# Optimization experiments

Hardware: AMD Instinct MI355X
Metric: run time of the kernel (lower is better)

The kernel has to match this reference:

```python
import jax, jax.numpy as jnp
import numpy as np

N_EMBD = 384
HEAD_SIZE = 16

def setup_inputs() -> dict:
    key = jax.random.key(0)
    k1, k2, k3, k4 = jax.random.split(key, 4)
    B, T = 4, 4096
    x = jax.random.normal(k1, (B, T, N_EMBD), dtype=jnp.float32)
    # nn.Linear(n_embd, head_size, bias=False): y = x @ W^T, W: [head_size, n_embd].
    # Store transposed [n_embd, head_size] for direct matmul.
    s = 1.0 / np.sqrt(N_EMBD)
    Wk = jax.random.uniform(k2, (N_EMBD, HEAD_SIZE), jnp.float32, -s, s)
    Wq = jax.random.uniform(k3, (N_EMBD, HEAD_SIZE), jnp.float32, -s, s)
    Wv = jax.random.uniform(k4, (N_EMBD, HEAD_SIZE), jnp.float32, -s, s)
    return {"x": x, "Wk": Wk, "Wq": Wq, "Wv": Wv}

def reference(x, Wk, Wq, Wv):
    B, T, C = x.shape
    k = x @ Wk  # [B,T,H]
    q = x @ Wq
    v = x @ Wv
    scale = k.shape[-1] ** -0.5
    wei = jnp.einsum('bth,bsh->bts', q, k) * scale  # [B,T,T]
    causal = jnp.tril(jnp.ones((T, T), dtype=bool))
    wei = jnp.where(causal, wei, -jnp.inf)
    wei = jax.nn.softmax(wei, axis=-1)
    out = jnp.einsum('bts,bsh->bth', wei, v)  # [B,T,H]
    return out
```

## Files before the change

kernel.cpp:

```cpp
#include <hip/hip_runtime.h>


constexpr int B_DIM = 4;
constexpr int T_SEQ = 4096;
constexpr int C_DIM = 384;
constexpr int H_DIM = 16;
constexpr int NROW  = B_DIM * T_SEQ;

typedef __bf16 bf16x8 __attribute__((ext_vector_type(8)));
typedef float  f32x4  __attribute__((ext_vector_type(4)));

__device__ __forceinline__ unsigned short f2bf(float f) {
  unsigned int u = __builtin_bit_cast(unsigned int, f);
  u += 0x7fffu + ((u >> 16) & 1u);
  return (unsigned short)(u >> 16);
}
__device__ __forceinline__ bf16x8 as_bf16x8(uint4 u) {
  return __builtin_bit_cast(bf16x8, u);
}

__global__ __launch_bounds__(256) void wconv(
    const float* __restrict__ Wk, const float* __restrict__ Wq,
    const float* __restrict__ Wv, unsigned short* __restrict__ WT) {
  const int i = blockIdx.x * 256 + threadIdx.x;
  const int m = i / 6144;
  const int r = i - m * 6144;
  const int n = r / 384;
  const int k = r - n * 384;
  const float* __restrict__ W = (m == 0) ? Wk : (m == 1) ? Wq : Wv;
  WT[i] = f2bf(W[k * 16 + n]);
}

__global__ __launch_bounds__(128) void qkv_mfma(
    const float* __restrict__ x, const unsigned short* __restrict__ WT,
    unsigned short* __restrict__ Kb,
    unsigned short* __restrict__ Qb,
    unsigned short* __restrict__ VTb)
{
  const int tid  = threadIdx.x;
  const int w    = tid >> 6;
  const int lane = tid & 63;
  const int quad = lane >> 4;
  const int col  = lane & 15;
  const int r0   = blockIdx.x << 4;
  const int kb   = w * 6;

  __shared__ float mrg[12][64];

  const float4* __restrict__ xp =
      reinterpret_cast<const float4*>(x + (size_t)(r0 + col) * C_DIM) + quad * 2;
  float4 araw[12];
#pragma unroll
  for (int kk = 0; kk < 6; ++kk) {
    araw[2 * kk]     = xp[(kb + kk) * 8];
    araw[2 * kk + 1] = xp[(kb + kk) * 8 + 1];
  }

  const uint4* __restrict__ bk = reinterpret_cast<const uint4*>(
      WT + (size_t)col * 384 + quad * 8);
  const uint4* __restrict__ bq = bk + 768;
  const uint4* __restrict__ bv = bk + 1536;

  f32x4 ck = {0.f, 0.f, 0.f, 0.f};
  f32x4 cq = {0.f, 0.f, 0.f, 0.f};
  f32x4 cv = {0.f, 0.f, 0.f, 0.f};
#pragma unroll
  for (int kk = 0; kk < 6; ++kk) {
    uint4 pk;
    const float4 a0 = araw[2 * kk], a1 = araw[2 * kk + 1];
    pk.x = (unsigned)f2bf(a0.x) | ((unsigned)f2bf(a0.y) << 16);
    pk.y = (unsigned)f2bf(a0.z) | ((unsigned)f2bf(a0.w) << 16);
    pk.z = (unsigned)f2bf(a1.x) | ((unsigned)f2bf(a1.y) << 16);
    pk.w = (unsigned)f2bf(a1.z) | ((unsigned)f2bf(a1.w) << 16);
    const bf16x8 av = as_bf16x8(pk);
    ck = __builtin_amdgcn_mfma_f32_16x16x32_bf16(av, as_bf16x8(bk[(kb + kk) * 4]), ck, 0, 0, 0);
    cq = __builtin_amdgcn_mfma_f32_16x16x32_bf16(av, as_bf16x8(bq[(kb + kk) * 4]), cq, 0, 0, 0);
    cv = __builtin_amdgcn_mfma_f32_16x16x32_bf16(av, as_bf16x8(bv[(kb + kk) * 4]), cv, 0, 0, 0);
  }

  if (w == 1) {
#pragma unroll
    for (int r = 0; r < 4; ++r) {
      mrg[r][lane]     = ck[r];
      mrg[4 + r][lane] = cq[r];
      mrg[8 + r][lane] = cv[r];
    }
  }
  __syncthreads();
  if (w == 0) {
    const float SC = 0.25f * 1.44269504088896341f;
#pragma unroll
    for (int r = 0; r < 4; ++r) {
      const float vk = ck[r] + mrg[r][lane];
      const float vq = cq[r] + mrg[4 + r][lane];
      const float vv = cv[r] + mrg[8 + r][lane];
      const int row = r0 + quad * 4 + r;
      Kb[row * 16 + col]      = f2bf(vk);
      Qb[row * 32 + col]      = f2bf(vq * SC);
      Qb[row * 32 + 16 + col] = 0;
      const int bb = row >> 12, t = row & 4095;
      VTb[(((size_t)(bb * 16 + col)) << 12) + t] = f2bf(vv);
    }
  }
}

__global__ __launch_bounds__(256) void flash_v4(
    const unsigned short* __restrict__ Qb,
    const unsigned short* __restrict__ Kb,
    const unsigned short* __restrict__ VTb,
    float* __restrict__ out)
{
  const int tid  = threadIdx.x;
  const int w    = tid >> 6;
  const int lane = tid & 63;
  const int quad = lane >> 4;
  const int col  = lane & 15;
  const int b    = blockIdx.x & 3;
  const int qt   = 255 - (blockIdx.x >> 2);
  const int r0   = qt << 4;

  __shared__ __attribute__((aligned(16))) unsigned short Pl[4][2][16 * 72];
  __shared__ float mrg[4][8][64];

  const uint4* qp = reinterpret_cast<const uint4*>(
      Qb + (((size_t)(b * T_SEQ + r0 + col)) << 5) + quad * 8);
  const bf16x8 qa = as_bf16x8(qp[0]);

  f32x4 o = {0.f, 0.f, 0.f, 0.f};
  float l_[4] = {0.f, 0.f, 0.f, 0.f};

  const unsigned short* Kbase = Kb + ((size_t)(b * T_SEQ) << 4);
  const unsigned short* Vbase = VTb + (((size_t)(b * 16 + col)) << 12);
  const int nch = (qt + 4) >> 2;

  unsigned short* const P0 = Pl[w][0];
  unsigned short* const P1 = Pl[w][1];

  auto computeP = [&](int c, unsigned short* P) {
    const int kt0 = c << 2;
    f32x4 sf[4];
#pragma unroll
    for (int t = 0; t < 4; ++t) {
      const int kt = kt0 + t;
      if (kt <= qt) {
        const uint4* kp = reinterpret_cast<const uint4*>(
            Kbase + (((size_t)(kt * 16 + col)) << 4) + quad * 8);
        f32x4 z = {0.f, 0.f, 0.f, 0.f};
        sf[t] = __builtin_amdgcn_mfma_f32_16x16x32_bf16(qa, as_bf16x8(kp[0]), z, 0, 0, 0);
      } else {
#pragma unroll
        for (int r = 0; r < 4; ++r) sf[t][r] = -1e30f;
      }
    }
    const int td = qt - kt0;
    if (td >= 0 && td < 4) {
#pragma unroll
      for (int r = 0; r < 4; ++r)
        if (col > quad * 4 + r) sf[td][r] = -1e30f;
    }
#pragma unroll
    for (int t = 0; t < 4; ++t) {
#pragma unroll
      for (int r = 0; r < 4; ++r) {
        const float p = __builtin_amdgcn_exp2f(sf[t][r]);
        l_[r] += p;
        P[(quad * 4 + r) * 72 + t * 16 + col] = f2bf(p);
      }
    }
  };

  auto doPV = [&](int c, const unsigned short* P) {
    const uint4 v0 = *reinterpret_cast<const uint4*>(Vbase + c * 64 + quad * 8);
    const uint4 v1 = *reinterpret_cast<const uint4*>(Vbase + c * 64 + 32 + quad * 8);
    const uint4 p0 = *reinterpret_cast<const uint4*>(P + col * 72 + quad * 8);
    const uint4 p1 = *reinterpret_cast<const uint4*>(P + col * 72 + 32 + quad * 8);
    o = __builtin_amdgcn_mfma_f32_16x16x32_bf16(as_bf16x8(p0), as_bf16x8(v0), o, 0, 0, 0);
    o = __builtin_amdgcn_mfma_f32_16x16x32_bf16(as_bf16x8(p1), as_bf16x8(v1), o, 0, 0, 0);
  };

  int c = w;
  if (c < nch) {
    computeP(c, P0);
    int last = c; c += 4;
    while (c < nch) {
      computeP(c, P1);
      doPV(last, P0);
      last = c; c += 4;
      if (c >= nch) { doPV(last, P1); last = -1; break; }
      computeP(c, P0);
      doPV(last, P1);
      last = c; c += 4;
    }
    if (last >= 0) doPV(last, P0);
  }

#pragma unroll
  for (int d = 1; d < 16; d <<= 1) {
#pragma unroll
    for (int r = 0; r < 4; ++r) l_[r] += __shfl_xor(l_[r], d, 16);
  }

#pragma unroll
  for (int r = 0; r < 4; ++r) {
    mrg[w][r][lane]     = l_[r];
    mrg[w][4 + r][lane] = o[r];
  }
  __syncthreads();
  if (w == 0) {
#pragma unroll
    for (int r = 0; r < 4; ++r) {
      const float L = mrg[0][r][lane] + mrg[1][r][lane] +
                      mrg[2][r][lane] + mrg[3][r][lane];
      const float O = mrg[0][4 + r][lane] + mrg[1][4 + r][lane] +
                      mrg[2][4 + r][lane] + mrg[3][4 + r][lane];
      out[(((size_t)(b * T_SEQ + r0 + quad * 4 + r)) << 4) + col] = O / L;
    }
  }
}

extern "C" void kernel_launch(void* const* d_in, const int* in_sizes, int n_in,
                              void* d_out, int out_size, void* d_ws, size_t ws_size,
                              hipStream_t stream) {
  const float* x  = (const float*)d_in[0];
  const float* Wk = (const float*)d_in[1];
  const float* Wq = (const float*)d_in[2];
  const float* Wv = (const float*)d_in[3];
  float* outp = (float*)d_out;

  unsigned short* Qb  = (unsigned short*)d_ws;
  unsigned short* Kb  = Qb + (size_t)NROW * 32;
  unsigned short* VTb = Kb + (size_t)NROW * 16 + 64;
  unsigned short* WT  = VTb + (size_t)NROW * 16;

  wconv<<<72, 256, 0, stream>>>(Wk, Wq, Wv, WT);
  qkv_mfma<<<1024, 128, 0, stream>>>(x, WT, Kb, Qb, VTb);
  flash_v4<<<B_DIM * 256, 256, 0, stream>>>(Qb, Kb, VTb, outp);
}
```

Measured before the change: 109.2 us.

## Split each causal query tile across two blocks and merge partials in a separate kernel

```diff
diff --git a/kernel.cpp b/kernel.cpp
--- a/kernel.cpp
+++ b/kernel.cpp
@@ -104,23 +104,24 @@
   }
 }
 
-__global__ __launch_bounds__(256) void flash_v4(
+__global__ __launch_bounds__(256) void flash_v5(
     const unsigned short* __restrict__ Qb,
     const unsigned short* __restrict__ Kb,
     const unsigned short* __restrict__ VTb,
-    float* __restrict__ out)
+    float* __restrict__ PO, float* __restrict__ PL)
 {
   const int tid  = threadIdx.x;
   const int w    = tid >> 6;
   const int lane = tid & 63;
   const int quad = lane >> 4;
   const int col  = lane & 15;
-  const int b    = blockIdx.x & 3;
-  const int qt   = 255 - (blockIdx.x >> 2);
+  const int qt   = 255 - (blockIdx.x >> 3);
+  const int b    = (blockIdx.x >> 1) & 3;
+  const int h    = blockIdx.x & 1;
+  const int slot = h * 4 + w;
   const int r0   = qt << 4;
 
   __shared__ __attribute__((aligned(16))) unsigned short Pl[4][2][16 * 72];
-  __shared__ float mrg[4][8][64];
 
   const uint4* qp = reinterpret_cast<const uint4*>(
       Qb + (((size_t)(b * T_SEQ + r0 + col)) << 5) + quad * 8);
@@ -178,18 +179,18 @@
     o = __builtin_amdgcn_mfma_f32_16x16x32_bf16(as_bf16x8(p1), as_bf16x8(v1), o, 0, 0, 0);
   };
 
-  int c = w;
+  int c = slot;
   if (c < nch) {
     computeP(c, P0);
-    int last = c; c += 4;
+    int last = c; c += 8;
     while (c < nch) {
       computeP(c, P1);
       doPV(last, P0);
-      last = c; c += 4;
+      last = c; c += 8;
       if (c >= nch) { doPV(last, P1); last = -1; break; }
       computeP(c, P0);
       doPV(last, P1);
-      last = c; c += 4;
+      last = c; c += 8;
     }
     if (last >= 0) doPV(last, P0);
   }
@@ -200,22 +201,28 @@
     for (int r = 0; r < 4; ++r) l_[r] += __shfl_xor(l_[r], d, 16);
   }
 
+  const size_t rowbase = (size_t)b * T_SEQ + r0;
+  float* pO = PO + ((size_t)slot * NROW + rowbase) * 16;
 #pragma unroll
   for (int r = 0; r < 4; ++r) {
-    mrg[w][r][lane]     = l_[r];
-    mrg[w][4 + r][lane] = o[r];
-  }
-  __syncthreads();
-  if (w == 0) {
-#pragma unroll
-    for (int r = 0; r < 4; ++r) {
-      const float L = mrg[0][r][lane] + mrg[1][r][lane] +
-                      mrg[2][r][lane] + mrg[3][r][lane];
-      const float O = mrg[0][4 + r][lane] + mrg[1][4 + r][lane] +
-                      mrg[2][4 + r][lane] + mrg[3][4 + r][lane];
-      out[(((size_t)(b * T_SEQ + r0 + quad * 4 + r)) << 4) + col] = O / L;
-    }
-  }
+    pO[(quad * 4 + r) * 16 + col] = o[r];
+    if (col == 0) PL[(size_t)slot * NROW + rowbase + quad * 4 + r] = l_[r];
+  }
+}
+
+__global__ __launch_bounds__(256) void flash_merge(
+    const float* __restrict__ PO, const float* __restrict__ PL,
+    float* __restrict__ out)
+{
+  const int i   = blockIdx.x * 256 + threadIdx.x;
+  const int row = i >> 4;
+  float O = 0.f, L = 0.f;
+#pragma unroll
+  for (int s = 0; s < 8; ++s) {
+    O += PO[((size_t)s * NROW) * 16 + i];
+    L += PL[(size_t)s * NROW + row];
+  }
+  out[i] = O / L;
 }
 
 extern "C" void kernel_launch(void* const* d_in, const int* in_sizes, int n_in,
@@ -231,8 +238,11 @@
   unsigned short* Kb  = Qb + (size_t)NROW * 32;
   unsigned short* VTb = Kb + (size_t)NROW * 16 + 64;
   unsigned short* WT  = VTb + (size_t)NROW * 16;
+  float* PO = (float*)(WT + 18432);
+  float* PL = PO + (size_t)8 * NROW * 16;
 
   wconv<<<72, 256, 0, stream>>>(Wk, Wq, Wv, WT);
   qkv_mfma<<<1024, 128, 0, stream>>>(x, WT, Kb, Qb, VTb);
-  flash_v4<<<B_DIM * 256, 256, 0, stream>>>(Qb, Kb, VTb, outp);
-}
+  flash_v5<<<2048, 256, 0, stream>>>(Qb, Kb, VTb, PO, PL);
+  flash_merge<<<1024, 256, 0, stream>>>(PO, PL, outp);
+}
```

Measured after the change: 104.0 us. 4.7% less time.
